# Kernel tuning notes

Hardware: AMD Instinct MI355X
Metric: run time of the kernel (lower is better)

## Reference

```python
import jax, jax.numpy as jnp
import numpy as np

D_MODEL = 768
M_DIM = 256
N_HEADS = 4
B, N = 16, 4096


def _l2norm(v):
    # F.normalize(dim=-1): v / max(||v||, 1e-12)
    return v / jnp.maximum(jnp.linalg.norm(v, axis=-1, keepdims=True), 1e-12)


def setup_inputs() -> dict:
    key = jax.random.key(0)
    ks = jax.random.split(key, 16)
    x = jax.random.normal(ks[0], (B, N, D_MODEL), dtype=jnp.float32)
    # frozen random projections (std 1.0 / 0.5 / 0.1), torch Linear weight layout [out, in]
    Wr1 = jax.random.normal(ks[1], (M_DIM, D_MODEL), dtype=jnp.float32) * 1.0
    Wr2 = jax.random.normal(ks[2], (M_DIM, D_MODEL), dtype=jnp.float32) * 0.5
    Wr3 = jax.random.normal(ks[3], (M_DIM, D_MODEL), dtype=jnp.float32) * 0.1
    # learned projection + LayerNorm
    Wl = jax.random.normal(ks[4], (M_DIM, D_MODEL), dtype=jnp.float32) * 0.02
    bl = jnp.zeros((M_DIM,), jnp.float32)
    ln_g = jnp.ones((M_DIM,), jnp.float32)
    ln_b = jnp.zeros((M_DIM,), jnp.float32)
    # MultiheadAttention in-proj (q,k,v) and out-proj
    Wq = jax.random.normal(ks[5], (M_DIM, M_DIM), dtype=jnp.float32) * 0.02
    Wk = jax.random.normal(ks[6], (M_DIM, M_DIM), dtype=jnp.float32) * 0.02
    Wv = jax.random.normal(ks[7], (M_DIM, M_DIM), dtype=jnp.float32) * 0.02
    bq = jnp.zeros((M_DIM,), jnp.float32)
    bk = jnp.zeros((M_DIM,), jnp.float32)
    bv = jnp.zeros((M_DIM,), jnp.float32)
    Wo = jax.random.normal(ks[8], (M_DIM, M_DIM), dtype=jnp.float32) * 0.02
    bo = jnp.zeros((M_DIM,), jnp.float32)
    return {"x": x, "Wr1": Wr1, "Wr2": Wr2, "Wr3": Wr3, "Wl": Wl, "bl": bl,
            "ln_g": ln_g, "ln_b": ln_b, "Wq": Wq, "bq": bq, "Wk": Wk, "bk": bk,
            "Wv": Wv, "bv": bv, "Wo": Wo, "bo": bo}


def reference(x, Wr1, Wr2, Wr3, Wl, bl, ln_g, ln_b, Wq, bq, Wk, bk, Wv, bv, Wo, bo):
    Bx, Nx, D = x.shape
    T = Bx * Nx
    xf = x.reshape(T, D)
    # three frozen random-projection branches, each L2-normalized
    r1 = _l2norm(xf @ Wr1.T)
    r2 = _l2norm(xf @ Wr2.T)
    r3 = _l2norm(xf @ Wr3.T)
    # learned branch: Linear -> LayerNorm (dropout is identity in eval) -> normalize
    h = xf @ Wl.T + bl
    mu = jnp.mean(h, axis=-1, keepdims=True)
    var = jnp.var(h, axis=-1, keepdims=True)
    h = (h - mu) / jnp.sqrt(var + 1e-5) * ln_g + ln_b
    lf = _l2norm(h)
    feats = jnp.stack([r1, r2, r3, lf], axis=1)  # [T, 4, M]
    q = jnp.mean(feats, axis=1, keepdims=True)   # [T, 1, M]
    M = feats.shape[-1]
    hd = M // N_HEADS
    qh = (q @ Wq.T + bq).reshape(T, 1, N_HEADS, hd)
    kh = (feats @ Wk.T + bk).reshape(T, 4, N_HEADS, hd)
    vh = (feats @ Wv.T + bv).reshape(T, 4, N_HEADS, hd)
    scores = jnp.einsum('tqhd,tkhd->thqk', qh, kh) / jnp.sqrt(jnp.float32(hd))
    attn = jax.nn.softmax(scores, axis=-1)       # softmax over the 4 branches
    fused = jnp.einsum('thqk,tkhd->tqhd', attn, vh).reshape(T, M)
    out = fused @ Wo.T + bo
    return _l2norm(out).reshape(Bx, Nx, M)
```

## Files before the change

kernel.cpp:

```cpp
#include <hip/hip_runtime.h>
#include <stdint.h>

#define TOK 65536
#define DMODEL 768

typedef short  s16x8 __attribute__((ext_vector_type(8)));
typedef __bf16 bf16x8 __attribute__((ext_vector_type(8)));
typedef float  f32x4 __attribute__((ext_vector_type(4)));

__device__ __forceinline__ float b2f(unsigned short u) {
  union { unsigned int i; float f; } v; v.i = ((unsigned int)u) << 16; return v.f;
}
__device__ __forceinline__ unsigned short f2b(float f) {
  union { float f; unsigned int i; } v; v.f = f;
  unsigned int r = v.i + 0x7fffu + ((v.i >> 16) & 1u);
  return (unsigned short)(r >> 16);
}
__device__ __forceinline__ float wsum(float v) {
#pragma unroll
  for (int off = 32; off >= 1; off >>= 1) v += __shfl_xor(v, off, 64);
  return v;
}

template <bool BF16_OUT, bool HAS_BIAS>
__global__ void gemm_bt(const unsigned short* __restrict__ A,
                        const unsigned short* __restrict__ W,
                        void* __restrict__ Cv,
                        const float* __restrict__ bias,
                        int M, int N, int K) {
  __shared__ __align__(16) unsigned short As[128 * 64];
  __shared__ __align__(16) unsigned short Bs[128 * 64];
  const int tid  = threadIdx.x;
  const int lane = tid & 63;
  const int w    = tid >> 6;
  const int wr   = w >> 1, wc = w & 1;
  const int l16  = lane & 15, lh = lane >> 4;
  const long arow0 = (long)blockIdx.x * 128;
  const long bcol0 = (long)blockIdx.y * 128;

  f32x4 acc[4][4];
#pragma unroll
  for (int mi = 0; mi < 4; ++mi)
#pragma unroll
    for (int ni = 0; ni < 4; ++ni) acc[mi][ni] = f32x4{0.f, 0.f, 0.f, 0.f};

  for (int k0 = 0; k0 < K; k0 += 64) {
#pragma unroll
    for (int i = 0; i < 4; ++i) {
      int sec = i * 4 + w;
      int row = sec * 8 + (lane >> 3);
      int col = (lane & 7) * 8;
      const unsigned short* ga = A + (arow0 + row) * (long)K + k0 + col;
      const unsigned short* gb = W + (bcol0 + row) * (long)K + k0 + col;
      __builtin_amdgcn_global_load_lds(
          (const __attribute__((address_space(1))) void*)ga,
          (__attribute__((address_space(3))) void*)&As[sec * 512], 16, 0, 0);
      __builtin_amdgcn_global_load_lds(
          (const __attribute__((address_space(1))) void*)gb,
          (__attribute__((address_space(3))) void*)&Bs[sec * 512], 16, 0, 0);
    }
    __syncthreads();
#pragma unroll
    for (int kk = 0; kk < 2; ++kk) {
      bf16x8 af[4], bf[4];
#pragma unroll
      for (int mi = 0; mi < 4; ++mi)
        af[mi] = __builtin_bit_cast(bf16x8,
            *(const s16x8*)&As[(wr * 64 + mi * 16 + l16) * 64 + kk * 32 + lh * 8]);
#pragma unroll
      for (int ni = 0; ni < 4; ++ni)
        bf[ni] = __builtin_bit_cast(bf16x8,
            *(const s16x8*)&Bs[(wc * 64 + ni * 16 + l16) * 64 + kk * 32 + lh * 8]);
#pragma unroll
      for (int mi = 0; mi < 4; ++mi)
#pragma unroll
        for (int ni = 0; ni < 4; ++ni)
          acc[mi][ni] = __builtin_amdgcn_mfma_f32_16x16x32_bf16(af[mi], bf[ni], acc[mi][ni], 0, 0, 0);
    }
    __syncthreads();
  }

#pragma unroll
  for (int mi = 0; mi < 4; ++mi)
#pragma unroll
    for (int ni = 0; ni < 4; ++ni)
#pragma unroll
      for (int j = 0; j < 4; ++j) {
        long row = arow0 + wr * 64 + mi * 16 + lh * 4 + j;
        long col = bcol0 + wc * 64 + ni * 16 + l16;
        float v = acc[mi][ni][j];
        if (HAS_BIAS) v += bias[col];
        if (BF16_OUT) ((unsigned short*)Cv)[row * N + col] = f2b(v);
        else          ((float*)Cv)[row * N + col] = v;
      }
}

__global__ void cast_x_kernel(const float* __restrict__ x, unsigned short* __restrict__ xb) {
  long i = ((long)blockIdx.x * 256 + threadIdx.x) * 4;
  float4 v = *reinterpret_cast<const float4*>(x + i);
  ushort4 o = {f2b(v.x), f2b(v.y), f2b(v.z), f2b(v.w)};
  *reinterpret_cast<ushort4*>(xb + i) = o;
}

__global__ void prep_wall_kernel(const float* __restrict__ Wr1, const float* __restrict__ Wr2,
                                 const float* __restrict__ Wr3, const float* __restrict__ Wl,
                                 unsigned short* __restrict__ Wall) {
  int idx = blockIdx.x * 256 + threadIdx.x;
  int base = idx * 4;
  int n = base / DMODEL, k = base % DMODEL;
  const float* src = (n < 256)  ? Wr1 + (long)n * DMODEL
                   : (n < 512)  ? Wr2 + (long)(n - 256) * DMODEL
                   : (n < 768)  ? Wr3 + (long)(n - 512) * DMODEL
                                : Wl  + (long)(n - 768) * DMODEL;
  float4 v = *reinterpret_cast<const float4*>(src + k);
  ushort4 o = {f2b(v.x), f2b(v.y), f2b(v.z), f2b(v.w)};
  *reinterpret_cast<ushort4*>(Wall + base) = o;
}

__global__ void prep_G_kernel(const float* __restrict__ Wq, const float* __restrict__ Wk,
                              const float* __restrict__ bq, unsigned short* __restrict__ Wg,
                              float* __restrict__ dvec) {
  int idx = blockIdx.x * 256 + threadIdx.x;
  int n = idx >> 8, a = idx & 255;
  int h = n >> 8, b = n & 255;
  const float* wq = Wq + (long)(h * 64) * 256 + a;
  const float* wk = Wk + (long)(h * 64) * 256 + b;
  float s = 0.f;
  for (int d = 0; d < 64; ++d) s += wq[d * 256] * wk[d * 256];
  Wg[(long)n * 256 + a] = f2b(s);
  if (a == 0) {
    float t = 0.f;
    const float* bqh = bq + h * 64;
    for (int d = 0; d < 64; ++d) t += bqh[d] * wk[d * 256];
    dvec[n] = t;
  }
}

__global__ void prep_P_kernel(const float* __restrict__ Wo, const float* __restrict__ Wv,
                              const float* __restrict__ bv, const float* __restrict__ bo,
                              unsigned short* __restrict__ Wp, float* __restrict__ bo2) {
  int idx = blockIdx.x * 256 + threadIdx.x;
  int m = idx >> 10, n = idx & 1023;
  int h = n >> 8, b = n & 255;
  const float* wo = Wo + (long)m * 256 + h * 64;
  const float* wv = Wv + (long)(h * 64) * 256 + b;
  float s = 0.f;
  for (int d = 0; d < 64; ++d) s += wo[d] * wv[d * 256];
  Wp[(long)m * 1024 + n] = f2b(s);
  if (n == 0) {
    float t = bo[m];
    const float* wor = Wo + (long)m * 256;
    for (int j = 0; j < 256; ++j) t += wor[j] * bv[j];
    bo2[m] = t;
  }
}

__global__ void norm_kernel(unsigned short* __restrict__ H, unsigned short* __restrict__ q,
                            const float* __restrict__ bl, const float* __restrict__ lng,
                            const float* __restrict__ lnb) {
  int token = blockIdx.x * 4 + (threadIdx.x >> 6);
  int lane = threadIdx.x & 63;
  unsigned short* row = H + (long)token * 1024;
  int b0 = lane * 4;
  float h[4][4];
#pragma unroll
  for (int s = 0; s < 4; ++s) {
    ushort4 v = *reinterpret_cast<const ushort4*>(row + s * 256 + b0);
    h[s][0] = b2f(v.x); h[s][1] = b2f(v.y); h[s][2] = b2f(v.z); h[s][3] = b2f(v.w);
  }
  float4 blv = *reinterpret_cast<const float4*>(bl + b0);
  h[3][0] += blv.x; h[3][1] += blv.y; h[3][2] += blv.z; h[3][3] += blv.w;

  float ss0 = 0, ss1 = 0, ss2 = 0, s3 = 0, ss3 = 0;
#pragma unroll
  for (int j = 0; j < 4; ++j) {
    ss0 += h[0][j] * h[0][j];
    ss1 += h[1][j] * h[1][j];
    ss2 += h[2][j] * h[2][j];
    s3  += h[3][j];
    ss3 += h[3][j] * h[3][j];
  }
  ss0 = wsum(ss0); ss1 = wsum(ss1); ss2 = wsum(ss2); s3 = wsum(s3); ss3 = wsum(ss3);
  float i0 = 1.f / fmaxf(sqrtf(ss0), 1e-12f);
  float i1 = 1.f / fmaxf(sqrtf(ss1), 1e-12f);
  float i2 = 1.f / fmaxf(sqrtf(ss2), 1e-12f);
  float mu = s3 * (1.f / 256.f);
  float var = ss3 * (1.f / 256.f) - mu * mu;
  float is = rsqrtf(var + 1e-5f);
  float4 gv = *reinterpret_cast<const float4*>(lng + b0);
  float4 bv = *reinterpret_cast<const float4*>(lnb + b0);
  float hn[4];
  hn[0] = (h[3][0] - mu) * is * gv.x + bv.x;
  hn[1] = (h[3][1] - mu) * is * gv.y + bv.y;
  hn[2] = (h[3][2] - mu) * is * gv.z + bv.z;
  hn[3] = (h[3][3] - mu) * is * gv.w + bv.w;
  float ssn = hn[0]*hn[0] + hn[1]*hn[1] + hn[2]*hn[2] + hn[3]*hn[3];
  ssn = wsum(ssn);
  float i3 = 1.f / fmaxf(sqrtf(ssn), 1e-12f);

  float f0[4], f1[4], f2[4], f3[4], qv[4];
#pragma unroll
  for (int j = 0; j < 4; ++j) {
    f0[j] = h[0][j] * i0; f1[j] = h[1][j] * i1; f2[j] = h[2][j] * i2; f3[j] = hn[j] * i3;
    qv[j] = 0.25f * (f0[j] + f1[j] + f2[j] + f3[j]);
  }
  ushort4 o0 = {f2b(f0[0]), f2b(f0[1]), f2b(f0[2]), f2b(f0[3])};
  ushort4 o1 = {f2b(f1[0]), f2b(f1[1]), f2b(f1[2]), f2b(f1[3])};
  ushort4 o2 = {f2b(f2[0]), f2b(f2[1]), f2b(f2[2]), f2b(f2[3])};
  ushort4 o3 = {f2b(f3[0]), f2b(f3[1]), f2b(f3[2]), f2b(f3[3])};
  ushort4 oq = {f2b(qv[0]), f2b(qv[1]), f2b(qv[2]), f2b(qv[3])};
  *reinterpret_cast<ushort4*>(row + 0 * 256 + b0) = o0;
  *reinterpret_cast<ushort4*>(row + 1 * 256 + b0) = o1;
  *reinterpret_cast<ushort4*>(row + 2 * 256 + b0) = o2;
  *reinterpret_cast<ushort4*>(row + 3 * 256 + b0) = o3;
  *reinterpret_cast<ushort4*>(q + (long)token * 256 + b0) = oq;
}

__global__ void attn_kernel(unsigned short* __restrict__ U, const unsigned short* __restrict__ F) {
  int token = blockIdx.x * 4 + (threadIdx.x >> 6);
  int lane = threadIdx.x & 63;
  unsigned short* urow = U + (long)token * 1024;
  const unsigned short* frow = F + (long)token * 1024;
  int b0 = lane * 4;
  float u[4][4], f[4][4];
#pragma unroll
  for (int s = 0; s < 4; ++s) {
    ushort4 uv = *reinterpret_cast<const ushort4*>(urow + s * 256 + b0);
    ushort4 fv = *reinterpret_cast<const ushort4*>(frow + s * 256 + b0);
    u[s][0] = b2f(uv.x); u[s][1] = b2f(uv.y); u[s][2] = b2f(uv.z); u[s][3] = b2f(uv.w);
    f[s][0] = b2f(fv.x); f[s][1] = b2f(fv.y); f[s][2] = b2f(fv.z); f[s][3] = b2f(fv.w);
  }
  float sc[4][4];
#pragma unroll
  for (int h = 0; h < 4; ++h)
#pragma unroll
    for (int k = 0; k < 4; ++k) {
      float s = 0.f;
#pragma unroll
      for (int j = 0; j < 4; ++j) s += u[h][j] * f[k][j];
      sc[h][k] = wsum(s);
    }
  float g[4][4];
#pragma unroll
  for (int h = 0; h < 4; ++h) {
    float m = fmaxf(fmaxf(sc[h][0], sc[h][1]), fmaxf(sc[h][2], sc[h][3]));
    float e0 = __expf((sc[h][0] - m) * 0.125f);
    float e1 = __expf((sc[h][1] - m) * 0.125f);
    float e2 = __expf((sc[h][2] - m) * 0.125f);
    float e3 = __expf((sc[h][3] - m) * 0.125f);
    float inv = 1.f / (e0 + e1 + e2 + e3);
#pragma unroll
    for (int j = 0; j < 4; ++j)
      g[h][j] = (e0 * f[0][j] + e1 * f[1][j] + e2 * f[2][j] + e3 * f[3][j]) * inv;
  }
#pragma unroll
  for (int h = 0; h < 4; ++h) {
    ushort4 o = {f2b(g[h][0]), f2b(g[h][1]), f2b(g[h][2]), f2b(g[h][3])};
    *reinterpret_cast<ushort4*>(urow + h * 256 + b0) = o;
  }
}

__global__ void l2_out_kernel(const float* __restrict__ in, float* __restrict__ out) {
  int token = blockIdx.x * 4 + (threadIdx.x >> 6);
  int lane = threadIdx.x & 63;
  float4 v = reinterpret_cast<const float4*>(in + (long)token * 256)[lane];
  float ss = wsum(v.x * v.x + v.y * v.y + v.z * v.z + v.w * v.w);
  float inv = 1.f / fmaxf(sqrtf(ss), 1e-12f);
  float4 o = {v.x * inv, v.y * inv, v.z * inv, v.w * inv};
  reinterpret_cast<float4*>(out + (long)token * 256)[lane] = o;
}

extern "C" void kernel_launch(void* const* d_in, const int* in_sizes, int n_in,
                              void* d_out, int out_size, void* d_ws, size_t ws_size,
                              hipStream_t stream) {
  const float* x   = (const float*)d_in[0];
  const float* Wr1 = (const float*)d_in[1];
  const float* Wr2 = (const float*)d_in[2];
  const float* Wr3 = (const float*)d_in[3];
  const float* Wl  = (const float*)d_in[4];
  const float* bl  = (const float*)d_in[5];
  const float* lng = (const float*)d_in[6];
  const float* lnb = (const float*)d_in[7];
  const float* Wq  = (const float*)d_in[8];
  const float* bq  = (const float*)d_in[9];
  const float* Wk  = (const float*)d_in[10];
  const float* Wv  = (const float*)d_in[12];
  const float* bv  = (const float*)d_in[13];
  const float* Wo  = (const float*)d_in[14];
  const float* bo  = (const float*)d_in[15];

  char* ws = (char*)d_ws;
  size_t off = 0;
  auto alloc = [&](size_t bytes) -> void* {
    void* p = ws + off;
    off += (bytes + 255) & ~(size_t)255;
    return p;
  };
  unsigned short* xbf  = (unsigned short*)alloc((size_t)TOK * DMODEL * 2);
  unsigned short* H    = (unsigned short*)alloc((size_t)TOK * 1024 * 2);
  unsigned short* qb   = (unsigned short*)alloc((size_t)TOK * 256 * 2);
  unsigned short* U    = (unsigned short*)alloc((size_t)TOK * 1024 * 2);
  unsigned short* Wall = (unsigned short*)alloc((size_t)1024 * DMODEL * 2);
  unsigned short* Wg   = (unsigned short*)alloc((size_t)1024 * 256 * 2);
  unsigned short* Wp   = (unsigned short*)alloc((size_t)256 * 1024 * 2);
  float* dvec = (float*)alloc(1024 * 4);
  float* bo2  = (float*)alloc(256 * 4);
  float* outpre = (float*)xbf;

  cast_x_kernel<<<(TOK * DMODEL) / 1024, 256, 0, stream>>>(x, xbf);
  prep_wall_kernel<<<(1024 * DMODEL) / 1024, 256, 0, stream>>>(Wr1, Wr2, Wr3, Wl, Wall);
  prep_G_kernel<<<1024, 256, 0, stream>>>(Wq, Wk, (const float*)d_in[9], Wg, dvec);
  prep_P_kernel<<<1024, 256, 0, stream>>>(Wo, Wv, bv, bo, Wp, bo2);

  gemm_bt<true, false><<<dim3(512, 8), 256, 0, stream>>>(xbf, Wall, H, nullptr, TOK, 1024, DMODEL);
  norm_kernel<<<TOK / 4, 256, 0, stream>>>(H, qb, bl, lng, lnb);
  gemm_bt<true, true><<<dim3(512, 8), 256, 0, stream>>>(qb, Wg, U, dvec, TOK, 1024, 256);
  attn_kernel<<<TOK / 4, 256, 0, stream>>>(U, H);
  gemm_bt<false, true><<<dim3(512, 2), 256, 0, stream>>>(U, Wp, outpre, bo2, TOK, 256, 1024);
  l2_out_kernel<<<TOK / 4, 256, 0, stream>>>(outpre, (float*)d_out);

  (void)in_sizes; (void)n_in; (void)out_size; (void)ws_size; (void)bq;
}
```

Measured before the change: 724.9 us.

## Swizzle GEMM LDS tiles and remap workgroups for XCD-aware L2 locality

The GEMM now stages tiles into LDS with an XOR-swizzled column layout and reads them back through the same swizzle, so the MFMA operand reads stop colliding on LDS banks. It also switches from a 2D grid to a 1D grid that is remapped so consecutive logical tiles go to the same XCD (bid&7 picks the chunk), and tiles sharing A rows stay together to reuse L2. The tile-to-output mapping moves into a runtime tile count parameter. The prep_G call uses bq directly, a cosmetic change.

```diff
diff --git a/kernel.cpp b/kernel.cpp
--- a/kernel.cpp
+++ b/kernel.cpp
@@ -27,7 +27,7 @@
                         const unsigned short* __restrict__ W,
                         void* __restrict__ Cv,
                         const float* __restrict__ bias,
-                        int M, int N, int K) {
+                        int M, int N, int K, int nt) {
   __shared__ __align__(16) unsigned short As[128 * 64];
   __shared__ __align__(16) unsigned short Bs[128 * 64];
   const int tid  = threadIdx.x;
@@ -35,23 +35,29 @@
   const int w    = tid >> 6;
   const int wr   = w >> 1, wc = w & 1;
   const int l16  = lane & 15, lh = lane >> 4;
-  const long arow0 = (long)blockIdx.x * 128;
-  const long bcol0 = (long)blockIdx.y * 128;
+
+  const int per = gridDim.x >> 3;
+  const int bid = blockIdx.x;
+  const int wg  = (bid & 7) * per + (bid >> 3);
+  const long arow0 = (long)(wg / nt) * 128;
+  const long bcol0 = (long)(wg % nt) * 128;
 
   f32x4 acc[4][4];
 #pragma unroll
   for (int mi = 0; mi < 4; ++mi)
 #pragma unroll
     for (int ni = 0; ni < 4; ++ni) acc[mi][ni] = f32x4{0.f, 0.f, 0.f, 0.f};
+
+  const int srow = lane >> 3;
+  const int scol = ((lane & 7) ^ (srow & 7)) * 8;
 
   for (int k0 = 0; k0 < K; k0 += 64) {
 #pragma unroll
     for (int i = 0; i < 4; ++i) {
       int sec = i * 4 + w;
-      int row = sec * 8 + (lane >> 3);
-      int col = (lane & 7) * 8;
-      const unsigned short* ga = A + (arow0 + row) * (long)K + k0 + col;
-      const unsigned short* gb = W + (bcol0 + row) * (long)K + k0 + col;
+      int row = sec * 8 + srow;
+      const unsigned short* ga = A + (arow0 + row) * (long)K + k0 + scol;
+      const unsigned short* gb = W + (bcol0 + row) * (long)K + k0 + scol;
       __builtin_amdgcn_global_load_lds(
           (const __attribute__((address_space(1))) void*)ga,
           (__attribute__((address_space(3))) void*)&As[sec * 512], 16, 0, 0);
@@ -63,14 +69,15 @@
 #pragma unroll
     for (int kk = 0; kk < 2; ++kk) {
       bf16x8 af[4], bf[4];
+      const int sw = (l16 & 7) << 3;
 #pragma unroll
       for (int mi = 0; mi < 4; ++mi)
         af[mi] = __builtin_bit_cast(bf16x8,
-            *(const s16x8*)&As[(wr * 64 + mi * 16 + l16) * 64 + kk * 32 + lh * 8]);
+            *(const s16x8*)&As[(((wr * 64 + mi * 16 + l16) * 64) + kk * 32 + lh * 8) ^ sw]);
 #pragma unroll
       for (int ni = 0; ni < 4; ++ni)
         bf[ni] = __builtin_bit_cast(bf16x8,
-            *(const s16x8*)&Bs[(wc * 64 + ni * 16 + l16) * 64 + kk * 32 + lh * 8]);
+            *(const s16x8*)&Bs[(((wc * 64 + ni * 16 + l16) * 64) + kk * 32 + lh * 8) ^ sw]);
 #pragma unroll
       for (int mi = 0; mi < 4; ++mi)
 #pragma unroll
@@ -309,15 +316,15 @@
 
   cast_x_kernel<<<(TOK * DMODEL) / 1024, 256, 0, stream>>>(x, xbf);
   prep_wall_kernel<<<(1024 * DMODEL) / 1024, 256, 0, stream>>>(Wr1, Wr2, Wr3, Wl, Wall);
-  prep_G_kernel<<<1024, 256, 0, stream>>>(Wq, Wk, (const float*)d_in[9], Wg, dvec);
+  prep_G_kernel<<<1024, 256, 0, stream>>>(Wq, Wk, bq, Wg, dvec);
   prep_P_kernel<<<1024, 256, 0, stream>>>(Wo, Wv, bv, bo, Wp, bo2);
 
-  gemm_bt<true, false><<<dim3(512, 8), 256, 0, stream>>>(xbf, Wall, H, nullptr, TOK, 1024, DMODEL);
+  gemm_bt<true, false><<<4096, 256, 0, stream>>>(xbf, Wall, H, nullptr, TOK, 1024, DMODEL, 8);
   norm_kernel<<<TOK / 4, 256, 0, stream>>>(H, qb, bl, lng, lnb);
-  gemm_bt<true, true><<<dim3(512, 8), 256, 0, stream>>>(qb, Wg, U, dvec, TOK, 1024, 256);
+  gemm_bt<true, true><<<4096, 256, 0, stream>>>(qb, Wg, U, dvec, TOK, 1024, 256, 8);
   attn_kernel<<<TOK / 4, 256, 0, stream>>>(U, H);
-  gemm_bt<false, true><<<dim3(512, 2), 256, 0, stream>>>(U, Wp, outpre, bo2, TOK, 256, 1024);
+  gemm_bt<false, true><<<1024, 256, 0, stream>>>(U, Wp, outpre, bo2, TOK, 256, 1024, 2);
   l2_out_kernel<<<TOK / 4, 256, 0, stream>>>(outpre, (float*)d_out);
 
-  (void)in_sizes; (void)n_in; (void)out_size; (void)ws_size; (void)bq;
-}
+  (void)in_sizes; (void)n_in; (void)out_size; (void)ws_size;
+}
```

After: 728.9 us. About the same (+0.6%).
